# Performance work log

Hardware: AMD Instinct MI355X
Metric: run time of the kernel (lower is better)

## Reference

```python
import jax, jax.numpy as jnp
import numpy as np

ALPHA_MIN = float(np.exp(-1.0 / 5.0))   # balance=False lower clamp
ALPHA_MAX = float(np.exp(-1.0 / 25.0))  # balance=False upper clamp


@jax.custom_vjp
def spike(u, thr):
    # Heaviside forward: spike if membrane potential exceeds threshold
    return (u > thr).astype(u.dtype)

def _spike_fwd(u, thr):
    return spike(u, thr), (u, thr)

def _spike_bwd(res, g):
    u, thr = res
    # Boxcar surrogate gradient: pass-through within +-0.5 of threshold
    mask = ((u > thr - 0.5) & (u <= thr + 0.5)).astype(g.dtype)
    return (g * mask, jnp.zeros_like(thr))

spike.defvjp(_spike_fwd, _spike_bwd)


def setup_inputs() -> dict:
    key = jax.random.key(0)
    kx, kw, kv, ka = jax.random.split(key, 4)
    B, T, I, H = 32, 1000, 256, 512
    x = jax.random.normal(kx, (B, T, I), dtype=jnp.float32)
    # W ~ U(-sqrt(1/I), sqrt(1/I)) as in nn.init.uniform_
    lim = float(np.sqrt(1.0 / I))
    W = jax.random.uniform(kw, (H, I), minval=-lim, maxval=lim, dtype=jnp.float32)
    # V: orthogonal init
    V = jnp.linalg.qr(jax.random.normal(kv, (H, H), dtype=jnp.float32))[0]
    alpha = jax.random.uniform(ka, (H,), minval=ALPHA_MIN, maxval=ALPHA_MAX, dtype=jnp.float32)
    v_thresh = jnp.ones((H,), dtype=jnp.float32)
    return {"x": x, "W": W, "V": V, "alpha": alpha, "v_thresh": v_thresh}


def reference(x, W, V, alpha, v_thresh):
    # x: [B, T, I]; W: [H, I]; V: [H, H]; alpha, v_thresh: [H]
    a = jnp.clip(alpha, ALPHA_MIN, ALPHA_MAX)
    H = V.shape[0]
    Vz = V * (1.0 - jnp.eye(H, dtype=V.dtype))  # fill_diagonal_(0)
    Wx = jnp.einsum('bti,hi->bth', x, W)        # feedforward drive [B,T,H]

    B = x.shape[0]
    ut0 = jnp.zeros((B, H), dtype=x.dtype)
    st0 = jnp.zeros((B, H), dtype=x.dtype)

    def step(carry, wx_t):
        ut, st = carry
        # leaky integration with recurrent spikes (fix_w_rec=False path)
        ut = a * (ut - st) + (1.0 - a) * (wx_t + st @ Vz)
        st = spike(ut, v_thresh)
        return (ut, st), st

    _, s = jax.lax.scan(step, (ut0, st0), jnp.swapaxes(Wx, 0, 1))  # [T,B,H]
    return jnp.swapaxes(s, 0, 1)  # [B,T,H]
```

## Files before the change

kernel.cpp:

```cpp
#include <hip/hip_runtime.h>

#define BATCH 32
#define TSTEPS 1000
#define KDIM 256
#define HDIM 512
#define NSEG 8
#define SEGL 125
#define SPFD 25

#define ALPHA_MIN_F 0.8187307530779818f
#define ALPHA_MAX_F 0.9607894391523232f

typedef __attribute__((ext_vector_type(8))) short bf16x8;
typedef __attribute__((ext_vector_type(8))) unsigned short u16x8;
typedef __attribute__((ext_vector_type(4))) float f32x4;

static __device__ __forceinline__ unsigned short f2bf(float f) {
  unsigned u = __float_as_uint(f);
  u += 0x7FFF + ((u >> 16) & 1);
  return (unsigned short)(u >> 16);
}
static __device__ __forceinline__ float bf2f(unsigned short s) {
  return __uint_as_float(((unsigned)s) << 16);
}

__global__ void init_fs(int* fs) {
  if (threadIdx.x < BATCH) fs[threadIdx.x] = TSTEPS;
}

__global__ __launch_bounds__(256) void cast_pack(const float* __restrict__ src,
                                                 unsigned short* __restrict__ hi,
                                                 unsigned short* __restrict__ lo,
                                                 int ntiles) {
  const int tile = blockIdx.x * 4 + (threadIdx.x >> 6);
  if (tile >= ntiles) return;
  const int lane = threadIdx.x & 63;
  const int row = tile * 16 + (lane & 15);
  const int kg = lane >> 4;
  const float* sp = src + (size_t)row * KDIM + kg * 8;
  unsigned short* hp = hi + (size_t)tile * 8 * 512 + lane * 8;
  unsigned short* lp = lo + (size_t)tile * 8 * 512 + lane * 8;
#pragma unroll
  for (int ks = 0; ks < 8; ++ks) {
    float4 a = *reinterpret_cast<const float4*>(sp + ks * 32);
    float4 b = *reinterpret_cast<const float4*>(sp + ks * 32 + 4);
    u16x8 h, l;
    h[0] = f2bf(a.x); l[0] = f2bf(a.x - bf2f(h[0]));
    h[1] = f2bf(a.y); l[1] = f2bf(a.y - bf2f(h[1]));
    h[2] = f2bf(a.z); l[2] = f2bf(a.z - bf2f(h[2]));
    h[3] = f2bf(a.w); l[3] = f2bf(a.w - bf2f(h[3]));
    h[4] = f2bf(b.x); l[4] = f2bf(b.x - bf2f(h[4]));
    h[5] = f2bf(b.y); l[5] = f2bf(b.y - bf2f(h[5]));
    h[6] = f2bf(b.z); l[6] = f2bf(b.z - bf2f(h[6]));
    h[7] = f2bf(b.w); l[7] = f2bf(b.w - bf2f(h[7]));
    *reinterpret_cast<u16x8*>(hp + ks * 512) = h;
    *reinterpret_cast<u16x8*>(lp + ks * 512) = l;
  }
}

__global__ __launch_bounds__(256, 1) void gemm_mfma(
    const float* __restrict__ x, const unsigned short* __restrict__ wph,
    const unsigned short* __restrict__ wpl, float* __restrict__ wx) {
  __shared__ short bsh[2][2][4096];
  const int tid = threadIdx.x;
  const int lane = tid & 63;
  const int wid = tid >> 6;
  const int row = lane & 15;
  const int kg = lane >> 4;
  const int tmb = blockIdx.x * 8 + wid * 2;
  const int m0 = tmb * 16;
  const int tO = tid * 8;

  bf16x8 ah[2][8], al[2][8];
#pragma unroll
  for (int rt = 0; rt < 2; ++rt) {
    const float* xp = x + (size_t)((tmb + rt) * 16 + row) * KDIM + kg * 8;
#pragma unroll
    for (int ks = 0; ks < 8; ++ks) {
      float4 f0 = *reinterpret_cast<const float4*>(xp + ks * 32);
      float4 f1 = *reinterpret_cast<const float4*>(xp + ks * 32 + 4);
      bf16x8 hv, lv;
      hv[0] = (short)f2bf(f0.x); lv[0] = (short)f2bf(f0.x - bf2f(hv[0]));
      hv[1] = (short)f2bf(f0.y); lv[1] = (short)f2bf(f0.y - bf2f(hv[1]));
      hv[2] = (short)f2bf(f0.z); lv[2] = (short)f2bf(f0.z - bf2f(hv[2]));
      hv[3] = (short)f2bf(f0.w); lv[3] = (short)f2bf(f0.w - bf2f(hv[3]));
      hv[4] = (short)f2bf(f1.x); lv[4] = (short)f2bf(f1.x - bf2f(hv[4]));
      hv[5] = (short)f2bf(f1.y); lv[5] = (short)f2bf(f1.y - bf2f(hv[5]));
      hv[6] = (short)f2bf(f1.z); lv[6] = (short)f2bf(f1.z - bf2f(hv[6]));
      hv[7] = (short)f2bf(f1.w); lv[7] = (short)f2bf(f1.w - bf2f(hv[7]));
      ah[rt][ks] = hv;
      al[rt][ks] = lv;
    }
  }

  {
    *reinterpret_cast<bf16x8*>(&bsh[0][0][tO]) =
        *reinterpret_cast<const bf16x8*>(wph + tO);
    *reinterpret_cast<bf16x8*>(&bsh[0][0][2048 + tO]) =
        *reinterpret_cast<const bf16x8*>(wph + 2048 + tO);
    *reinterpret_cast<bf16x8*>(&bsh[0][1][tO]) =
        *reinterpret_cast<const bf16x8*>(wpl + tO);
    *reinterpret_cast<bf16x8*>(&bsh[0][1][2048 + tO]) =
        *reinterpret_cast<const bf16x8*>(wpl + 2048 + tO);
  }
  __syncthreads();

  for (int ct = 0; ct < 32; ++ct) {
    const int buf = ct & 1;
    bf16x8 nh0, nh1, nl0, nl1;
    const bool pre = (ct < 31);
    if (pre) {
      const unsigned short* sh = wph + (size_t)(ct + 1) * 4096;
      const unsigned short* sl = wpl + (size_t)(ct + 1) * 4096;
      nh0 = *reinterpret_cast<const bf16x8*>(sh + tO);
      nh1 = *reinterpret_cast<const bf16x8*>(sh + 2048 + tO);
      nl0 = *reinterpret_cast<const bf16x8*>(sl + tO);
      nl1 = *reinterpret_cast<const bf16x8*>(sl + 2048 + tO);
    }

    f32x4 acc0 = {0.f, 0.f, 0.f, 0.f};
    f32x4 acc1 = {0.f, 0.f, 0.f, 0.f};
#pragma unroll
    for (int ks = 0; ks < 8; ++ks) {
      bf16x8 bh = *reinterpret_cast<const bf16x8*>(&bsh[buf][0][ks * 512 + lane * 8]);
      bf16x8 bl = *reinterpret_cast<const bf16x8*>(&bsh[buf][1][ks * 512 + lane * 8]);
      acc0 = __builtin_amdgcn_mfma_f32_16x16x32_bf16(ah[0][ks], bh, acc0, 0, 0, 0);
      acc1 = __builtin_amdgcn_mfma_f32_16x16x32_bf16(ah[1][ks], bh, acc1, 0, 0, 0);
      acc0 = __builtin_amdgcn_mfma_f32_16x16x32_bf16(al[0][ks], bh, acc0, 0, 0, 0);
      acc1 = __builtin_amdgcn_mfma_f32_16x16x32_bf16(al[1][ks], bh, acc1, 0, 0, 0);
      acc0 = __builtin_amdgcn_mfma_f32_16x16x32_bf16(ah[0][ks], bl, acc0, 0, 0, 0);
      acc1 = __builtin_amdgcn_mfma_f32_16x16x32_bf16(ah[1][ks], bl, acc1, 0, 0, 0);
    }
    const int n0 = ct * 16;
#pragma unroll
    for (int j = 0; j < 4; ++j) {
      wx[(size_t)(m0 + kg * 4 + j) * HDIM + n0 + row] = acc0[j];
      wx[(size_t)(m0 + 16 + kg * 4 + j) * HDIM + n0 + row] = acc1[j];
    }
    if (pre) {
      *reinterpret_cast<bf16x8*>(&bsh[buf ^ 1][0][tO]) = nh0;
      *reinterpret_cast<bf16x8*>(&bsh[buf ^ 1][0][2048 + tO]) = nh1;
      *reinterpret_cast<bf16x8*>(&bsh[buf ^ 1][1][tO]) = nl0;
      *reinterpret_cast<bf16x8*>(&bsh[buf ^ 1][1][2048 + tO]) = nl1;
    }
    __syncthreads();
  }
}

__global__ __launch_bounds__(64) void seg_sum(const float* __restrict__ wx,
                                              const float* __restrict__ alpha,
                                              float* __restrict__ cbuf) {
  const int hb = blockIdx.x & 7;
  const int seg = (blockIdx.x >> 3) & 7;
  const int b = blockIdx.x >> 6;
  const int h = (hb << 6) + threadIdx.x;
  const float a = fminf(fmaxf(alpha[h], ALPHA_MIN_F), ALPHA_MAX_F);
  const float na = 1.0f - a;
  const float* wp = wx + ((size_t)b * TSTEPS + seg * SEGL) * HDIM + h;

  float pf[SPFD];
#pragma unroll
  for (int d = 0; d < SPFD; ++d) pf[d] = wp[(size_t)d * HDIM];

  float c = 0.f;
  for (int j0 = 0; j0 < SEGL; j0 += SPFD) {
#pragma unroll
    for (int js = 0; js < SPFD; ++js) {
      const int j = j0 + js;
      const float w = pf[js];
      int jp = j + SPFD;
      if (jp > SEGL - 1) jp = SEGL - 1;
      pf[js] = wp[(size_t)jp * HDIM];
      c = fmaf(a, c, na * w);
    }
  }
  cbuf[(size_t)seg * BATCH * HDIM + (size_t)b * HDIM + h] = c;
}

__global__ __launch_bounds__(64) void seg_scan(const float* __restrict__ wx,
                                               const float* __restrict__ alpha,
                                               const float* __restrict__ vthr,
                                               const float* __restrict__ cbuf,
                                               float* __restrict__ out,
                                               int* __restrict__ fs) {
  const int hb = blockIdx.x & 7;
  const int seg = (blockIdx.x >> 3) & 7;
  const int b = blockIdx.x >> 6;
  const int h = (hb << 6) + threadIdx.x;
  const float a = fminf(fmaxf(alpha[h], ALPHA_MIN_F), ALPHA_MAX_F);
  const float na = 1.0f - a;
  const float th = vthr[h];
  const int t0g = seg * SEGL;
  const float* wp = wx + ((size_t)b * TSTEPS + t0g) * HDIM + h;
  float* op = out + ((size_t)b * TSTEPS + t0g) * HDIM + h;

  float pf[SPFD];
#pragma unroll
  for (int d = 0; d < SPFD; ++d) pf[d] = wp[(size_t)d * HDIM];

  float aL = 1.0f;
  for (int i = 0; i < SEGL; ++i) aL *= a;
  float u = 0.f;
  for (int k = 0; k < seg; ++k)
    u = fmaf(aL, u, cbuf[(size_t)k * BATCH * HDIM + (size_t)b * HDIM + h]);

  float s = 0.f;
  int first = TSTEPS;
  for (int j0 = 0; j0 < SEGL; j0 += SPFD) {
#pragma unroll
    for (int js = 0; js < SPFD; ++js) {
      const int j = j0 + js;
      const float w = pf[js];
      int jp = j + SPFD;
      if (jp > SEGL - 1) jp = SEGL - 1;
      pf[js] = wp[(size_t)jp * HDIM];
      u = fmaf(a, u - s, na * w);
      s = (u > th) ? 1.0f : 0.0f;
      op[(size_t)j * HDIM] = s;
      if (s != 0.0f && first == TSTEPS) {
        first = t0g + j;
        atomicMin(&fs[b], first);
      }
    }
  }
}

static __device__ __forceinline__ void scan_body(const float* wxbuf,
                                                 const float* __restrict__ V,
                                                 const float* __restrict__ alpha,
                                                 const float* __restrict__ vthr,
                                                 float* out, int b) {
  const int l = threadIdx.x;
  const int h0 = 4 * l;
  const int h1 = 256 + 4 * l;

  float4 al0 = *reinterpret_cast<const float4*>(alpha + h0);
  float4 al1 = *reinterpret_cast<const float4*>(alpha + h1);
  float4 th0 = *reinterpret_cast<const float4*>(vthr + h0);
  float4 th1 = *reinterpret_cast<const float4*>(vthr + h1);
  float a[8] = {al0.x, al0.y, al0.z, al0.w, al1.x, al1.y, al1.z, al1.w};
  float th[8] = {th0.x, th0.y, th0.z, th0.w, th1.x, th1.y, th1.z, th1.w};
  float na[8], u[8], s[8], r[8];
#pragma unroll
  for (int j = 0; j < 8; ++j) {
    float c = fminf(fmaxf(a[j], ALPHA_MIN_F), ALPHA_MAX_F);
    a[j] = c; na[j] = 1.0f - c;
    u[j] = 0.f; s[j] = 0.f; r[j] = 0.f;
  }
  const float* wb = wxbuf + (size_t)b * TSTEPS * HDIM;
  float* ob = out + (size_t)b * TSTEPS * HDIM;
  float4 p0[4], p1[4];
#pragma unroll
  for (int d = 0; d < 4; ++d) {
    p0[d] = *reinterpret_cast<const float4*>(wb + (size_t)d * HDIM + h0);
    p1[d] = *reinterpret_cast<const float4*>(wb + (size_t)d * HDIM + h1);
  }
  for (int t0 = 0; t0 < TSTEPS; t0 += 4) {
#pragma unroll
    for (int ts = 0; ts < 4; ++ts) {
      const int t = t0 + ts;
      float w8[8] = {p0[ts].x, p0[ts].y, p0[ts].z, p0[ts].w,
                     p1[ts].x, p1[ts].y, p1[ts].z, p1[ts].w};
      int tpre = t + 4;
      if (tpre > TSTEPS - 1) tpre = TSTEPS - 1;
      p0[ts] = *reinterpret_cast<const float4*>(wb + (size_t)tpre * HDIM + h0);
      p1[ts] = *reinterpret_cast<const float4*>(wb + (size_t)tpre * HDIM + h1);
#pragma unroll
      for (int j = 0; j < 8; ++j) {
        float un = fmaf(a[j], u[j] - s[j], na[j] * (w8[j] + r[j]));
        u[j] = un;
        s[j] = (un > th[j]) ? 1.0f : 0.0f;
      }
      *reinterpret_cast<float4*>(ob + (size_t)t * HDIM + h0) =
          make_float4(s[0], s[1], s[2], s[3]);
      *reinterpret_cast<float4*>(ob + (size_t)t * HDIM + h1) =
          make_float4(s[4], s[5], s[6], s[7]);
      float ssum = s[0] + s[1] + s[2] + s[3] + s[4] + s[5] + s[6] + s[7];
      unsigned long long anym = __ballot(ssum != 0.0f);
      if (anym != 0ull) {
        unsigned long long mk[8];
#pragma unroll
        for (int j = 0; j < 8; ++j) mk[j] = __ballot(s[j] != 0.0f);
        float rr[8] = {0.f, 0.f, 0.f, 0.f, 0.f, 0.f, 0.f, 0.f};
#pragma unroll
        for (int j2 = 0; j2 < 8; ++j2) {
          unsigned long long m = mk[j2];
          while (m) {
            int src = __builtin_ctzll(m);
            m &= m - 1;
            int hin = (j2 < 4) ? (src * 4 + j2) : (256 + src * 4 + (j2 - 4));
            const float* vrow = V + (size_t)hin * HDIM;
            float4 v0 = *reinterpret_cast<const float4*>(vrow + h0);
            float4 v1 = *reinterpret_cast<const float4*>(vrow + h1);
            float vv[8] = {v0.x, v0.y, v0.z, v0.w, v1.x, v1.y, v1.z, v1.w};
#pragma unroll
            for (int j = 0; j < 8; ++j) {
              int hj = (j < 4) ? (h0 + j) : (h1 + j - 4);
              rr[j] += (hj == hin) ? 0.0f : vv[j];
            }
          }
        }
#pragma unroll
        for (int j = 0; j < 8; ++j) r[j] = rr[j];
      } else {
#pragma unroll
        for (int j = 0; j < 8; ++j) r[j] = 0.0f;
      }
    }
  }
}

__global__ __launch_bounds__(64) void fallback_scan(
    const float* wxbuf, const float* __restrict__ V,
    const float* __restrict__ alpha, const float* __restrict__ vthr,
    float* out, const int* __restrict__ fs) {
  const int b = blockIdx.x;
  if (fs[b] >= TSTEPS - 1) return;
  scan_body(wxbuf, V, alpha, vthr, out, b);
}

__global__ __launch_bounds__(64) void rlif_scan(const float* wxbuf,
                                                const float* __restrict__ V,
                                                const float* __restrict__ alpha,
                                                const float* __restrict__ vthr,
                                                float* out) {
  scan_body(wxbuf, V, alpha, vthr, out, blockIdx.x);
}

__global__ __launch_bounds__(256) void gemm_xwT(const float* __restrict__ x,
                                                const float* __restrict__ W,
                                                float* __restrict__ wx) {
  __shared__ float As[32][64];
  __shared__ float Bs[32][64];
  const int m0 = blockIdx.x * 64;
  const int n0 = blockIdx.y * 64;
  const int tid = threadIdx.x;
  const int tx = tid & 15;
  const int ty = tid >> 4;
  const int lr = tid >> 2;
  const int lk = (tid & 3) * 8;

  float acc[4][4] = {};
  for (int k0 = 0; k0 < KDIM; k0 += 32) {
    const float4* ap =
        reinterpret_cast<const float4*>(x + (size_t)(m0 + lr) * KDIM + k0 + lk);
    const float4* bp =
        reinterpret_cast<const float4*>(W + (size_t)(n0 + lr) * KDIM + k0 + lk);
    float4 a0 = ap[0], a1 = ap[1];
    float4 b0 = bp[0], b1 = bp[1];
    __syncthreads();
    As[lk + 0][lr] = a0.x; As[lk + 1][lr] = a0.y;
    As[lk + 2][lr] = a0.z; As[lk + 3][lr] = a0.w;
    As[lk + 4][lr] = a1.x; As[lk + 5][lr] = a1.y;
    As[lk + 6][lr] = a1.z; As[lk + 7][lr] = a1.w;
    Bs[lk + 0][lr] = b0.x; Bs[lk + 1][lr] = b0.y;
    Bs[lk + 2][lr] = b0.z; Bs[lk + 3][lr] = b0.w;
    Bs[lk + 4][lr] = b1.x; Bs[lk + 5][lr] = b1.y;
    Bs[lk + 6][lr] = b1.z; Bs[lk + 7][lr] = b1.w;
    __syncthreads();
#pragma unroll
    for (int k = 0; k < 32; ++k) {
      float4 av = *reinterpret_cast<const float4*>(&As[k][ty * 4]);
      float4 bv = *reinterpret_cast<const float4*>(&Bs[k][tx * 4]);
      float am[4] = {av.x, av.y, av.z, av.w};
      float bn[4] = {bv.x, bv.y, bv.z, bv.w};
#pragma unroll
      for (int i = 0; i < 4; ++i)
#pragma unroll
        for (int j = 0; j < 4; ++j) acc[i][j] = fmaf(am[i], bn[j], acc[i][j]);
    }
  }
#pragma unroll
  for (int i = 0; i < 4; ++i) {
    float4 o = make_float4(acc[i][0], acc[i][1], acc[i][2], acc[i][3]);
    *reinterpret_cast<float4*>(wx + (size_t)(m0 + ty * 4 + i) * HDIM + n0 +
                               tx * 4) = o;
  }
}

extern "C" void kernel_launch(void* const* d_in, const int* in_sizes, int n_in,
                              void* d_out, int out_size, void* d_ws,
                              size_t ws_size, hipStream_t stream) {
  const float* x = (const float*)d_in[0];
  const float* W = (const float*)d_in[1];
  const float* V = (const float*)d_in[2];
  const float* alpha = (const float*)d_in[3];
  const float* vthr = (const float*)d_in[4];
  float* out = (float*)d_out;

  const size_t wx_b = (size_t)BATCH * TSTEPS * HDIM * 4;
  const size_t wh_b = (size_t)HDIM * KDIM * 2;
  const size_t cb_b = (size_t)NSEG * BATCH * HDIM * 4;
  const size_t needA = wx_b + 2 * wh_b + cb_b + 128;
  const size_t needB = wx_b + cb_b + 128;

  char* ws = (char*)d_ws;
  if (ws_size >= needA) {
    float* wx = (float*)ws;
    unsigned short* wph = (unsigned short*)(ws + wx_b);
    unsigned short* wpl = wph + (size_t)HDIM * KDIM;
    float* cbuf = (float*)(ws + wx_b + 2 * wh_b);
    int* fs = (int*)(ws + wx_b + 2 * wh_b + cb_b);

    hipLaunchKernelGGL(init_fs, dim3(1), dim3(64), 0, stream, fs);
    hipLaunchKernelGGL(cast_pack, dim3(8), dim3(256), 0, stream, W, wph, wpl,
                       HDIM / 16);
    hipLaunchKernelGGL(gemm_mfma, dim3(BATCH * TSTEPS / 128), dim3(256), 0,
                       stream, x, wph, wpl, wx);
    hipLaunchKernelGGL(seg_sum, dim3(BATCH * NSEG * 8), dim3(64), 0, stream,
                       wx, alpha, cbuf);
    hipLaunchKernelGGL(seg_scan, dim3(BATCH * NSEG * 8), dim3(64), 0, stream,
                       wx, alpha, vthr, cbuf, out, fs);
    hipLaunchKernelGGL(fallback_scan, dim3(BATCH), dim3(64), 0, stream, wx, V,
                       alpha, vthr, out, fs);
  } else if (ws_size >= needB) {
    float* wx = (float*)ws;
    float* cbuf = (float*)(ws + wx_b);
    int* fs = (int*)(ws + wx_b + cb_b);
    hipLaunchKernelGGL(init_fs, dim3(1), dim3(64), 0, stream, fs);
    hipLaunchKernelGGL(gemm_xwT, dim3(BATCH * TSTEPS / 64, HDIM / 64),
                       dim3(256), 0, stream, x, W, wx);
    hipLaunchKernelGGL(seg_sum, dim3(BATCH * NSEG * 8), dim3(64), 0, stream,
                       wx, alpha, cbuf);
    hipLaunchKernelGGL(seg_scan, dim3(BATCH * NSEG * 8), dim3(64), 0, stream,
                       wx, alpha, vthr, cbuf, out, fs);
    hipLaunchKernelGGL(fallback_scan, dim3(BATCH), dim3(64), 0, stream, wx, V,
                       alpha, vthr, out, fs);
  } else {
    float* wx = (ws_size >= wx_b) ? (float*)ws : out;
    hipLaunchKernelGGL(gemm_xwT, dim3(BATCH * TSTEPS / 64, HDIM / 64),
                       dim3(256), 0, stream, x, W, wx);
    hipLaunchKernelGGL(rlif_scan, dim3(BATCH), dim3(64), 0, stream, wx, V,
                       alpha, vthr, out);
  }
}
```

Before: 84.35 us.

## Retile MFMA GEMM into N-quarter blocks with whole W slice resident in LDS

The GEMM kernel is restructured. Each block now covers a 128-column quarter of H (grid 125x4, 512 threads), loads its full bf16 hi/lo W slice into 128 KB of LDS once, and drops the per-column-tile double-buffered loop and its barriers. The x loads are issued before the W staging so they overlap it. Each of the three split-bf16 products gets its own accumulator, which shortens MFMA dependency chains. In exchange, x is now read and converted four times (once per N quarter), and the large LDS footprint limits how many blocks fit per CU despite launch_bounds(512,2).

```diff
diff --git a/kernel.cpp b/kernel.cpp
--- a/kernel.cpp
+++ b/kernel.cpp
@@ -58,92 +58,91 @@
   }
 }
 
-__global__ __launch_bounds__(256, 1) void gemm_mfma(
+__global__ __launch_bounds__(512, 2) void gemm_mfma2(
     const float* __restrict__ x, const unsigned short* __restrict__ wph,
     const unsigned short* __restrict__ wpl, float* __restrict__ wx) {
-  __shared__ short bsh[2][2][4096];
+  __shared__ unsigned short wlds[2][32768];
   const int tid = threadIdx.x;
   const int lane = tid & 63;
   const int wid = tid >> 6;
   const int row = lane & 15;
   const int kg = lane >> 4;
-  const int tmb = blockIdx.x * 8 + wid * 2;
-  const int m0 = tmb * 16;
-  const int tO = tid * 8;
+  const int nq = blockIdx.y;
+  const int p = blockIdx.x * 8 + wid;
+  const int m0 = p * 32;
+
+  f32x4 araw[2][16];
+#pragma unroll
+  for (int mt = 0; mt < 2; ++mt) {
+    const float* xp = x + (size_t)(m0 + mt * 16 + row) * KDIM + kg * 8;
+#pragma unroll
+    for (int ks = 0; ks < 8; ++ks) {
+      araw[mt][ks * 2 + 0] = *reinterpret_cast<const f32x4*>(xp + ks * 32);
+      araw[mt][ks * 2 + 1] = *reinterpret_cast<const f32x4*>(xp + ks * 32 + 4);
+    }
+  }
+
+  {
+    const unsigned short* sh = wph + (size_t)nq * 32768;
+    const unsigned short* sl = wpl + (size_t)nq * 32768;
+#pragma unroll
+    for (int r = 0; r < 8; ++r) {
+      const int o = (r * 512 + tid) * 8;
+      *reinterpret_cast<bf16x8*>(&wlds[0][o]) =
+          *reinterpret_cast<const bf16x8*>(sh + o);
+      *reinterpret_cast<bf16x8*>(&wlds[1][o]) =
+          *reinterpret_cast<const bf16x8*>(sl + o);
+    }
+  }
+  __syncthreads();
 
   bf16x8 ah[2][8], al[2][8];
 #pragma unroll
-  for (int rt = 0; rt < 2; ++rt) {
-    const float* xp = x + (size_t)((tmb + rt) * 16 + row) * KDIM + kg * 8;
+  for (int mt = 0; mt < 2; ++mt) {
 #pragma unroll
     for (int ks = 0; ks < 8; ++ks) {
-      float4 f0 = *reinterpret_cast<const float4*>(xp + ks * 32);
-      float4 f1 = *reinterpret_cast<const float4*>(xp + ks * 32 + 4);
+      f32x4 f0 = araw[mt][ks * 2 + 0];
+      f32x4 f1 = araw[mt][ks * 2 + 1];
       bf16x8 hv, lv;
-      hv[0] = (short)f2bf(f0.x); lv[0] = (short)f2bf(f0.x - bf2f(hv[0]));
-      hv[1] = (short)f2bf(f0.y); lv[1] = (short)f2bf(f0.y - bf2f(hv[1]));
-      hv[2] = (short)f2bf(f0.z); lv[2] = (short)f2bf(f0.z - bf2f(hv[2]));
-      hv[3] = (short)f2bf(f0.w); lv[3] = (short)f2bf(f0.w - bf2f(hv[3]));
-      hv[4] = (short)f2bf(f1.x); lv[4] = (short)f2bf(f1.x - bf2f(hv[4]));
-      hv[5] = (short)f2bf(f1.y); lv[5] = (short)f2bf(f1.y - bf2f(hv[5]));
-      hv[6] = (short)f2bf(f1.z); lv[6] = (short)f2bf(f1.z - bf2f(hv[6]));
-      hv[7] = (short)f2bf(f1.w); lv[7] = (short)f2bf(f1.w - bf2f(hv[7]));
-      ah[rt][ks] = hv;
-      al[rt][ks] = lv;
-    }
-  }
-
-  {
-    *reinterpret_cast<bf16x8*>(&bsh[0][0][tO]) =
-        *reinterpret_cast<const bf16x8*>(wph + tO);
-    *reinterpret_cast<bf16x8*>(&bsh[0][0][2048 + tO]) =
-        *reinterpret_cast<const bf16x8*>(wph + 2048 + tO);
-    *reinterpret_cast<bf16x8*>(&bsh[0][1][tO]) =
-        *reinterpret_cast<const bf16x8*>(wpl + tO);
-    *reinterpret_cast<bf16x8*>(&bsh[0][1][2048 + tO]) =
-        *reinterpret_cast<const bf16x8*>(wpl + 2048 + tO);
-  }
-  __syncthreads();
-
-  for (int ct = 0; ct < 32; ++ct) {
-    const int buf = ct & 1;
-    bf16x8 nh0, nh1, nl0, nl1;
-    const bool pre = (ct < 31);
-    if (pre) {
-      const unsigned short* sh = wph + (size_t)(ct + 1) * 4096;
-      const unsigned short* sl = wpl + (size_t)(ct + 1) * 4096;
-      nh0 = *reinterpret_cast<const bf16x8*>(sh + tO);
-      nh1 = *reinterpret_cast<const bf16x8*>(sh + 2048 + tO);
-      nl0 = *reinterpret_cast<const bf16x8*>(sl + tO);
-      nl1 = *reinterpret_cast<const bf16x8*>(sl + 2048 + tO);
-    }
-
-    f32x4 acc0 = {0.f, 0.f, 0.f, 0.f};
-    f32x4 acc1 = {0.f, 0.f, 0.f, 0.f};
+      hv[0] = (short)f2bf(f0[0]); lv[0] = (short)f2bf(f0[0] - bf2f(hv[0]));
+      hv[1] = (short)f2bf(f0[1]); lv[1] = (short)f2bf(f0[1] - bf2f(hv[1]));
+      hv[2] = (short)f2bf(f0[2]); lv[2] = (short)f2bf(f0[2] - bf2f(hv[2]));
+      hv[3] = (short)f2bf(f0[3]); lv[3] = (short)f2bf(f0[3] - bf2f(hv[3]));
+      hv[4] = (short)f2bf(f1[0]); lv[4] = (short)f2bf(f1[0] - bf2f(hv[4]));
+      hv[5] = (short)f2bf(f1[1]); lv[5] = (short)f2bf(f1[1] - bf2f(hv[5]));
+      hv[6] = (short)f2bf(f1[2]); lv[6] = (short)f2bf(f1[2] - bf2f(hv[6]));
+      hv[7] = (short)f2bf(f1[3]); lv[7] = (short)f2bf(f1[3] - bf2f(hv[7]));
+      ah[mt][ks] = hv;
+      al[mt][ks] = lv;
+    }
+  }
+
+#pragma unroll
+  for (int tl = 0; tl < 8; ++tl) {
+    f32x4 accA[2] = {{0.f, 0.f, 0.f, 0.f}, {0.f, 0.f, 0.f, 0.f}};
+    f32x4 accB[2] = {{0.f, 0.f, 0.f, 0.f}, {0.f, 0.f, 0.f, 0.f}};
+    f32x4 accC[2] = {{0.f, 0.f, 0.f, 0.f}, {0.f, 0.f, 0.f, 0.f}};
 #pragma unroll
     for (int ks = 0; ks < 8; ++ks) {
-      bf16x8 bh = *reinterpret_cast<const bf16x8*>(&bsh[buf][0][ks * 512 + lane * 8]);
-      bf16x8 bl = *reinterpret_cast<const bf16x8*>(&bsh[buf][1][ks * 512 + lane * 8]);
-      acc0 = __builtin_amdgcn_mfma_f32_16x16x32_bf16(ah[0][ks], bh, acc0, 0, 0, 0);
-      acc1 = __builtin_amdgcn_mfma_f32_16x16x32_bf16(ah[1][ks], bh, acc1, 0, 0, 0);
-      acc0 = __builtin_amdgcn_mfma_f32_16x16x32_bf16(al[0][ks], bh, acc0, 0, 0, 0);
-      acc1 = __builtin_amdgcn_mfma_f32_16x16x32_bf16(al[1][ks], bh, acc1, 0, 0, 0);
-      acc0 = __builtin_amdgcn_mfma_f32_16x16x32_bf16(ah[0][ks], bl, acc0, 0, 0, 0);
-      acc1 = __builtin_amdgcn_mfma_f32_16x16x32_bf16(ah[1][ks], bl, acc1, 0, 0, 0);
-    }
-    const int n0 = ct * 16;
-#pragma unroll
-    for (int j = 0; j < 4; ++j) {
-      wx[(size_t)(m0 + kg * 4 + j) * HDIM + n0 + row] = acc0[j];
-      wx[(size_t)(m0 + 16 + kg * 4 + j) * HDIM + n0 + row] = acc1[j];
-    }
-    if (pre) {
-      *reinterpret_cast<bf16x8*>(&bsh[buf ^ 1][0][tO]) = nh0;
-      *reinterpret_cast<bf16x8*>(&bsh[buf ^ 1][0][2048 + tO]) = nh1;
-      *reinterpret_cast<bf16x8*>(&bsh[buf ^ 1][1][tO]) = nl0;
-      *reinterpret_cast<bf16x8*>(&bsh[buf ^ 1][1][2048 + tO]) = nl1;
-    }
-    __syncthreads();
+      const int o = (tl * 8 + ks) * 512 + lane * 8;
+      bf16x8 bh = *reinterpret_cast<const bf16x8*>(&wlds[0][o]);
+      bf16x8 bl = *reinterpret_cast<const bf16x8*>(&wlds[1][o]);
+#pragma unroll
+      for (int mt = 0; mt < 2; ++mt) {
+        accA[mt] = __builtin_amdgcn_mfma_f32_16x16x32_bf16(ah[mt][ks], bh, accA[mt], 0, 0, 0);
+        accB[mt] = __builtin_amdgcn_mfma_f32_16x16x32_bf16(al[mt][ks], bh, accB[mt], 0, 0, 0);
+        accC[mt] = __builtin_amdgcn_mfma_f32_16x16x32_bf16(ah[mt][ks], bl, accC[mt], 0, 0, 0);
+      }
+    }
+    const int n0 = nq * 128 + tl * 16;
+#pragma unroll
+    for (int mt = 0; mt < 2; ++mt) {
+#pragma unroll
+      for (int j = 0; j < 4; ++j) {
+        wx[(size_t)(m0 + mt * 16 + kg * 4 + j) * HDIM + n0 + row] =
+            (accA[mt][j] + accB[mt][j]) + accC[mt][j];
+      }
+    }
   }
 }
 
@@ -405,8 +404,8 @@
     hipLaunchKernelGGL(init_fs, dim3(1), dim3(64), 0, stream, fs);
     hipLaunchKernelGGL(cast_pack, dim3(8), dim3(256), 0, stream, W, wph, wpl,
                        HDIM / 16);
-    hipLaunchKernelGGL(gemm_mfma, dim3(BATCH * TSTEPS / 128), dim3(256), 0,
-                       stream, x, wph, wpl, wx);
+    hipLaunchKernelGGL(gemm_mfma2, dim3(125, 4), dim3(512), 0, stream, x, wph,
+                       wpl, wx);
     hipLaunchKernelGGL(seg_sum, dim3(BATCH * NSEG * 8), dim3(64), 0, stream,
                        wx, alpha, cbuf);
     hipLaunchKernelGGL(seg_scan, dim3(BATCH * NSEG * 8), dim3(64), 0, stream,
```

Result: slower. 115.7 us (+37.2%).
